# Performance work log

Hardware: AMD Instinct MI355X
Metric: run time of the kernel (lower is better)

Reference implementation:

```python
import jax, jax.numpy as jnp
import numpy as np

MAXTIME = 1406073600
MINTIME = 832550400
SPAN = 10000
TIME_EMB = 100
N_GATE = 8
NUM_INTEREST = 4
DIM = 64
SEQ = 256
BATCH = 1024
ALPHA = 0.1
PI = 3.14159  # matches the literal in the source


def _build_time_table():
    # TimeEncoder: interleaved sin/cos positional table over time buckets.
    n = MAXTIME // SPAN + 3
    pos = np.arange(n, dtype=np.float64)[:, None]
    div = np.exp(np.arange(TIME_EMB // 2, dtype=np.float64) * -(np.log(10000.0) / TIME_EMB))[None, :]
    te = np.zeros((n, TIME_EMB), dtype=np.float32)
    te[:, 0::2] = np.sin(pos * div)
    te[:, 1::2] = np.cos(pos * div)
    return jnp.asarray(te)

_TIME_TABLE = _build_time_table()


def _time_encode(t):
    idx = (t / SPAN).astype(jnp.int32)
    return _TIME_TABLE[idx - jnp.min(idx)]


def setup_inputs() -> dict:
    key = jax.random.key(0)
    ks = jax.random.split(key, 11)
    B, S, D, NI, G = BATCH, SEQ, DIM, NUM_INTEREST, N_GATE
    item_his_emb = jax.random.normal(ks[0], (B, S, D), jnp.float32)
    item_eb = jax.random.normal(ks[1], (B, D), jnp.float32)
    # query times near maxtime, history times strictly earlier -> positive deltas
    t_batch = MAXTIME - 1e6 * jax.random.uniform(ks[2], (B,), jnp.float32)
    t_his = MINTIME + (MAXTIME - MINTIME - 1e6) * jax.random.uniform(ks[3], (B, S), jnp.float32)
    mask = (jax.random.uniform(ks[4], (B, S)) > 0.3).astype(jnp.float32)
    W1 = jax.random.normal(ks[5], (3 * TIME_EMB, 100), jnp.float32) / np.sqrt(3 * TIME_EMB)
    b1 = jnp.zeros((100,), jnp.float32)
    W2 = jax.random.normal(ks[6], (100, 1), jnp.float32) * 0.1
    b2 = jnp.zeros((1,), jnp.float32)
    phase = 100000.0 * jax.random.uniform(ks[7], (1, 1, G), jnp.float32)
    tao = 86400.0 * jnp.array([[[1, 2, 7, 14, 30, 60, 365, 730]]], jnp.float32)
    ratio = 0.3 * jax.random.uniform(ks[8], (1, 1, G), jnp.float32)
    gate_emb = jax.random.normal(ks[9], (1, D, G), jnp.float32)
    w_bilinear = jax.random.normal(ks[10], (S, NI * D, D), jnp.float32)
    return {"item_his_emb": item_his_emb, "item_eb": item_eb, "t_batch": t_batch,
            "t_his": t_his, "mask": mask, "W1": W1, "b1": b1, "W2": W2, "b2": b2,
            "phase": phase, "tao": tao, "ratio": ratio, "gate_emb": gate_emb,
            "w_bilinear": w_bilinear, "ta": 2}


def reference(item_his_emb, item_eb, t_batch, t_his, mask, W1, b1, W2, b2,
              phase, tao, ratio, gate_emb, w_bilinear, ta):
    B, S, D = item_his_emb.shape
    NI = NUM_INTEREST
    # --- time factor ---
    t_tiled = jnp.broadcast_to(t_batch[:, None], (B, S))
    time_feature = jnp.concatenate([_time_encode(t_tiled), _time_encode(t_his),
                                    _time_encode(t_tiled - t_his)], axis=2)  # [B,S,300]
    hidden1 = jax.nn.relu(time_feature @ W1 + b1)
    t_factor = jnp.transpose(jax.nn.sigmoid(hidden1 @ W2 + b2), (0, 2, 1))  # [B,1,S]
    # --- circadian gate factor ---
    phi = jnp.mod(t_his[:, :, None] - phase, tao) / tao  # [B,S,G]
    gate = jnp.where(phi < ratio, jnp.maximum(jnp.sin(PI * phi / ratio), 0.0), ALPHA * phi)
    gate_ratio = jax.nn.softmax(jnp.einsum('bsd,dg->bsg', item_his_emb, gate_emb[0]), axis=2) * gate
    g_factor = jnp.sum(gate_ratio, axis=2)[:, None, :]  # [B,1,S]
    reg1 = jnp.linalg.norm(t_factor)
    reg2 = jnp.linalg.norm(ratio) + jnp.linalg.norm(phase) / 100000.0
    # ta == 2 branch
    loss_reg = 0.1 * reg1 + 1.0 * reg2 + 1.0 / reg1 + 0.1 / reg2
    factor = jnp.broadcast_to(t_factor + g_factor, (B, NI, S))
    # --- bilinear_type == 2 projection ---
    item_emb_hat = jnp.einsum('skd,bsd->bsk', w_bilinear, item_his_emb)  # [B,S,NI*D]
    item_emb_hat = item_emb_hat.reshape(B, S, NI, D).transpose(0, 2, 1, 3)  # [B,NI,S,D]
    hat_iter = jax.lax.stop_gradient(item_emb_hat)
    # --- dynamic routing, 3 iterations ---
    cw = jnp.zeros((B, NI, S), item_his_emb.dtype)
    amask = mask[:, None, :]
    cap = None
    for i in range(3):
        sw = jax.nn.softmax(cw, axis=1)           # softmax over interests
        sw = jnp.where(amask == 0, 0.0, sw)
        src = hat_iter if i < 2 else item_emb_hat
        cap = jnp.einsum('bks,bksd->bkd', sw, src)  # [B,NI,D]
        n2 = jnp.sum(cap * cap, axis=-1, keepdims=True)
        cap = (n2 / (1.0 + n2) / jnp.sqrt(n2 + 1e-9)) * cap  # squash
        if i < 2:
            delta = jnp.einsum('bksd,bkd->bks', hat_iter, cap) * factor
            cw = cw + delta
    interest_capsule = cap  # [B,NI,D]
    # --- hard readout ---
    atten = jax.nn.softmax(jnp.einsum('bkd,bd->bk', interest_capsule, item_eb), axis=1)
    readout = interest_capsule[jnp.arange(B), jnp.argmax(atten, axis=1)]  # [B,D]
    return interest_capsule, readout, loss_reg
```

## Files before the change

kernel.cpp:

```cpp
#include <hip/hip_runtime.h>
#include <math.h>
#include <limits.h>

#define BB 1024
#define SS 256
#define DD 64
#define NI 4
#define NG 8
#define TE_N 100
#define PMAX 57420
#define ROWP 100
#define TPB 16

typedef _Float16 half8 __attribute__((ext_vector_type(8)));
typedef _Float16 half4 __attribute__((ext_vector_type(4)));
typedef float f32x4 __attribute__((ext_vector_type(4)));

#define OFF_FTH   ((size_t)0)
#define OFF_FDF   ((size_t)PMAX*ROWP)
#define OFF_GTB   ((size_t)2*PMAX*ROWP)
#define OFF_FAC   (OFF_GTB + (size_t)BB*ROWP)
#define OFF_SCAL  (OFF_FAC + (size_t)BB*SS)
#define OFF_HAT   (OFF_SCAL + 32)

__device__ inline float dpp_add_xor1(float x){
    int i = __builtin_bit_cast(int, x);
    int p = __builtin_amdgcn_update_dpp(i, i, 0xB1, 0xF, 0xF, true);
    return x + __builtin_bit_cast(float, p);
}
__device__ inline float dpp_add_xor2(float x){
    int i = __builtin_bit_cast(int, x);
    int p = __builtin_amdgcn_update_dpp(i, i, 0x4E, 0xF, 0xF, true);
    return x + __builtin_bit_cast(float, p);
}
__device__ inline float swz_add_xor16(float x){
    int i = __builtin_bit_cast(int, x);
    int p = __builtin_amdgcn_ds_swizzle(i, 0x401F);
    return x + __builtin_bit_cast(float, p);
}

__global__ void k_init(float* ws){
    if (threadIdx.x == 0){
        int* mi = (int*)(ws + OFF_SCAL);
        mi[0] = INT_MAX; mi[1] = INT_MAX; mi[2] = INT_MAX;
        ws[OFF_SCAL + 4] = 0.0f;
    }
}

__global__ void k_min(const float* __restrict__ tb, const float* __restrict__ th, float* ws){
    int gid = blockIdx.x * blockDim.x + threadIdx.x;
    int stride = gridDim.x * blockDim.x;
    int m0 = INT_MAX, m1 = INT_MAX, m2 = INT_MAX;
    for (int i = gid; i < BB*SS; i += stride){
        float t  = th[i];
        float t2 = tb[i >> 8];
        int i1 = (int)(t / 10000.0f);
        int i2 = (int)((t2 - t) / 10000.0f);
        m1 = min(m1, i1);
        m2 = min(m2, i2);
    }
    if (gid < BB) m0 = (int)(tb[gid] / 10000.0f);
    #pragma unroll
    for (int off = 1; off < 64; off <<= 1){
        m0 = min(m0, __shfl_xor(m0, off));
        m1 = min(m1, __shfl_xor(m1, off));
        m2 = min(m2, __shfl_xor(m2, off));
    }
    if ((threadIdx.x & 63) == 0){
        int* mi = (int*)(ws + OFF_SCAL);
        atomicMin(mi + 0, m0);
        atomicMin(mi + 1, m1);
        atomicMin(mi + 2, m2);
    }
}

__global__ void k_tables(const float* __restrict__ W1, float* ws){
    int pbase = blockIdx.x * TPB;
    int t = threadIdx.x;
    __shared__ float te[TPB][TE_N];
    for (int idx = t; idx < TPB*50; idx += 128){
        int pp = idx / 50, h = idx - pp*50;
        double div = exp((double)h * -0.09210340371976184);
        double a = (double)(pbase + pp) * div;
        te[pp][2*h]   = (float)sin(a);
        te[pp][2*h+1] = (float)cos(a);
    }
    __syncthreads();
    if (t < TE_N){
        float a1[TPB], a2[TPB];
        #pragma unroll
        for (int pp = 0; pp < TPB; pp++){ a1[pp] = 0.f; a2[pp] = 0.f; }
        for (int i = 0; i < TE_N; i++){
            float w1v = W1[(100+i)*100 + t];
            float w2v = W1[(200+i)*100 + t];
            #pragma unroll
            for (int pp = 0; pp < TPB; pp++){
                float v = te[pp][i];
                a1[pp] += v * w1v;
                a2[pp] += v * w2v;
            }
        }
        for (int pp = 0; pp < TPB; pp++){
            int p = pbase + pp;
            if (p < PMAX){
                ws[OFF_FTH + (size_t)p*ROWP + t] = a1[pp];
                ws[OFF_FDF + (size_t)p*ROWP + t] = a2[pp];
            }
        }
    }
}

__global__ void k_gtb(const float* __restrict__ tb, const float* __restrict__ W1,
                      const float* __restrict__ b1, float* ws){
    int b = blockIdx.x;
    int t = threadIdx.x;
    const int* mi = (const int*)(ws + OFF_SCAL);
    int p = (int)(tb[b] / 10000.0f) - mi[0];
    __shared__ float te[TE_N];
    if (t < TE_N/2){
        double div = exp((double)t * -0.09210340371976184);
        double a = (double)p * div;
        te[2*t]   = (float)sin(a);
        te[2*t+1] = (float)cos(a);
    }
    __syncthreads();
    if (t < TE_N){
        float a1 = b1[t];
        for (int i = 0; i < TE_N; i++) a1 += te[i] * W1[i*100 + t];
        ws[OFF_GTB + (size_t)b*ROWP + t] = a1;
    }
}

__global__ void __launch_bounds__(256) k_factor(const float* __restrict__ tbatch,
                         const float* __restrict__ th_, const float* __restrict__ W2,
                         const float* __restrict__ b2, float* ws){
    int b  = blockIdx.x >> 1;
    int sh = blockIdx.x & 1;
    int t  = threadIdx.x;
    int lane = t & 63, wv = t >> 6;
    __shared__ float sgtb[TE_N];
    if (t < TE_N) sgtb[t] = ws[OFF_GTB + (size_t)b*ROWP + t];
    __syncthreads();

    bool tail = (lane < 36);
    float w2a = W2[lane];
    float w2b = tail ? W2[64 + lane] : 0.f;
    float ga  = sgtb[lane];
    float gb  = tail ? sgtb[64 + lane] : 0.f;
    float bias = b2[0];

    int sbase = sh*128 + wv*32;
    const int* mi = (const int*)(ws + OFF_SCAL);
    int pth = 0, pdf = 0;
    if (lane < 32){
        float thv = th_[(size_t)b*SS + sbase + lane];
        float tbv = tbatch[b];
        pth = (int)(thv / 10000.0f) - mi[1];
        pdf = (int)((tbv - thv) / 10000.0f) - mi[2];
        pth = min(max(pth, 0), PMAX-1);
        pdf = min(max(pdf, 0), PMAX-1);
    }

    float tfkeep = 0.f;
    float r1acc  = 0.f;
    #pragma unroll 4
    for (int i = 0; i < 32; i++){
        int p1 = __shfl(pth, i);
        int p2 = __shfl(pdf, i);
        const float* r1 = ws + OFF_FTH + (size_t)p1*ROWP;
        const float* r2 = ws + OFF_FDF + (size_t)p2*ROWP;
        float a  = r1[lane];
        float c  = r2[lane];
        float a2 = tail ? r1[64 + lane] : 0.f;
        float c2 = tail ? r2[64 + lane] : 0.f;
        float h = fmaxf(ga + a + c, 0.f) * w2a;
        if (tail) h += fmaxf(gb + a2 + c2, 0.f) * w2b;
        #pragma unroll
        for (int off = 1; off < 64; off <<= 1) h += __shfl_xor(h, off);
        float tf = 1.f / (1.f + expf(-(h + bias)));
        if (lane == i){ tfkeep = tf; r1acc += tf*tf; }
    }
    if (lane < 32) ws[OFF_FAC + (size_t)b*SS + sbase + lane] = tfkeep;
    #pragma unroll
    for (int off = 1; off < 64; off <<= 1) r1acc += __shfl_xor(r1acc, off);
    if (lane == 0) atomicAdd(ws + OFF_SCAL + 4, r1acc);
}

__global__ void __launch_bounds__(256) k_gate(const float* __restrict__ X,
      const float* __restrict__ th_, const float* __restrict__ phase,
      const float* __restrict__ tao, const float* __restrict__ ratio,
      const float* __restrict__ ge, float* ws){
    __shared__ float sge[NG][DD];
    int t = threadIdx.x;
    for (int i = t; i < DD*NG; i += 256) sge[i & 7][i >> 3] = ge[i];
    __syncthreads();
    int gid = blockIdx.x * 256 + t;

    float lg[NG];
    #pragma unroll
    for (int g = 0; g < NG; g++) lg[g] = 0.f;
    const float4* xr = (const float4*)(X + (size_t)gid*DD);
    #pragma unroll 4
    for (int dc = 0; dc < 16; dc++){
        float4 xv = xr[dc];
        #pragma unroll
        for (int g = 0; g < NG; g++){
            lg[g] += xv.x*sge[g][dc*4+0] + xv.y*sge[g][dc*4+1]
                   + xv.z*sge[g][dc*4+2] + xv.w*sge[g][dc*4+3];
        }
    }
    float mx = lg[0];
    #pragma unroll
    for (int g = 1; g < NG; g++) mx = fmaxf(mx, lg[g]);
    float thv = th_[gid];
    float es = 0.f, gf = 0.f;
    #pragma unroll
    for (int g = 0; g < NG; g++){
        float e = expf(lg[g] - mx);
        es += e;
        float phv = fmodf(thv - phase[g], tao[g]) / tao[g];
        float gv = (phv < ratio[g]) ? fmaxf(sinf(3.14159f*phv/ratio[g]), 0.f) : 0.1f*phv;
        gf += e * gv;
    }
    ws[OFF_FAC + gid] += gf / es;
}

__global__ void __launch_bounds__(512, 2)
k_hat(const float* __restrict__ X, const float* __restrict__ Wb,
      float* __restrict__ hat, int b0, int nb){
    int btile = blockIdx.x;
    int s     = blockIdx.y;
    int t     = threadIdx.x;
    int rows = nb - btile*64; if (rows > 64) rows = 64;

    __shared__ _Float16 lds[40960];

    const float* xbase = X + ((size_t)(b0 + btile*64)*SS + s)*DD;
    #pragma unroll
    for (int i = 0; i < 2; i++){
        int q = t + 512*i;
        int r = q >> 4, jf = q & 15;
        float4 v;
        if (r < rows) v = *(const float4*)(xbase + (size_t)r*SS*DD + jf*4);
        else { v.x = 0.f; v.y = 0.f; v.z = 0.f; v.w = 0.f; }
        half4 h, l;
        h.x = (_Float16)v.x; h.y = (_Float16)v.y; h.z = (_Float16)v.z; h.w = (_Float16)v.w;
        l.x = (_Float16)(v.x - (float)h.x); l.y = (_Float16)(v.y - (float)h.y);
        l.z = (_Float16)(v.z - (float)h.z); l.w = (_Float16)(v.w - (float)h.w);
        int bt = r >> 4, rowin = r & 15;
        int j0 = jf*4;
        int kk = j0 >> 5, jb = (j0 & 31) >> 3, e0 = j0 & 7;
        int lane = rowin + 16*jb;
        int base = ((bt*2 + kk)*2)*512 + lane*8 + e0;
        *(half4*)(lds + base)       = h;
        *(half4*)(lds + base + 512) = l;
    }
    const float* wbase = Wb + (size_t)s*16384;
    #pragma unroll
    for (int i = 0; i < 8; i++){
        int q = t + 512*i;
        int kd = q >> 4, jf = q & 15;
        float4 v = *(const float4*)(wbase + kd*64 + jf*4);
        half4 h, l;
        h.x = (_Float16)v.x; h.y = (_Float16)v.y; h.z = (_Float16)v.z; h.w = (_Float16)v.w;
        l.x = (_Float16)(v.x - (float)h.x); l.y = (_Float16)(v.y - (float)h.y);
        l.z = (_Float16)(v.z - (float)h.z); l.w = (_Float16)(v.w - (float)h.w);
        int kdt = kd >> 4, rowin = kd & 15;
        int j0 = jf*4;
        int kk = j0 >> 5, jb = (j0 & 31) >> 3, e0 = j0 & 7;
        int lane = rowin + 16*jb;
        int base = 8192 + ((kdt*2 + kk)*2)*512 + lane*8 + e0;
        *(half4*)(lds + base)       = h;
        *(half4*)(lds + base + 512) = l;
    }
    __syncthreads();

    int w    = t >> 6;
    int lane = t & 63;
    int wbt  = w >> 1;
    int kdh  = w & 1;

    half8 a[2][2];
    #pragma unroll
    for (int kk = 0; kk < 2; kk++)
        #pragma unroll
        for (int hl = 0; hl < 2; hl++)
            a[kk][hl] = *(half8*)(lds + ((wbt*2 + kk)*2 + hl)*512 + lane*8);

    int brow = (lane >> 4) * 4;
    int bcol = lane & 15;

    #pragma unroll
    for (int kdti = 0; kdti < 8; kdti++){
        int kdt = kdh*8 + kdti;
        const _Float16* wb0 = lds + 8192 + ((kdt*2 + 0)*2)*512 + lane*8;
        const _Float16* wb1 = lds + 8192 + ((kdt*2 + 1)*2)*512 + lane*8;
        half8 bh0 = *(half8*)(wb0);
        half8 bl0 = *(half8*)(wb0 + 512);
        half8 bh1 = *(half8*)(wb1);
        half8 bl1 = *(half8*)(wb1 + 512);
        f32x4 acc = {0.f, 0.f, 0.f, 0.f};
        acc = __builtin_amdgcn_mfma_f32_16x16x32_f16(a[0][0], bh0, acc, 0, 0, 0);
        acc = __builtin_amdgcn_mfma_f32_16x16x32_f16(a[0][0], bl0, acc, 0, 0, 0);
        acc = __builtin_amdgcn_mfma_f32_16x16x32_f16(a[0][1], bh0, acc, 0, 0, 0);
        acc = __builtin_amdgcn_mfma_f32_16x16x32_f16(a[1][0], bh1, acc, 0, 0, 0);
        acc = __builtin_amdgcn_mfma_f32_16x16x32_f16(a[1][0], bl1, acc, 0, 0, 0);
        acc = __builtin_amdgcn_mfma_f32_16x16x32_f16(a[1][1], bh1, acc, 0, 0, 0);
        int kd = kdt*16 + bcol;
        #pragma unroll
        for (int r = 0; r < 4; r++){
            int rl = wbt*16 + brow + r;
            if (rl < rows)
                hat[((size_t)(btile*64 + rl)*SS + s)*256 + kd] = acc[r];
        }
    }
}

__global__ void __launch_bounds__(1024) k_route(const float* __restrict__ eb,
                                                const float* __restrict__ mask_,
                                                const float* __restrict__ ws,
                                                const float* __restrict__ hat,
                                                float* __restrict__ out, int b0){
    int bl = blockIdx.x;
    int b = b0 + bl;
    int t = threadIdx.x;
    int lane = t & 63, wv = t >> 6;
    int k = (lane >> 2) & 3;
    int s_local = (lane & 3) | (((lane >> 4) & 3) << 2);
    int s = wv * 16 + s_local;
    __shared__ float part[16][4][64];
    __shared__ float capl[4][68];
    __shared__ float logits[4];
    __shared__ int kms;

    float hat_r[64];
    const float4* hsrc = (const float4*)(hat + (size_t)bl*65536 + ((size_t)s*4 + k)*64);
    #pragma unroll
    for (int jc = 0; jc < 16; jc++){
        float4 v = hsrc[jc];
        hat_r[4*jc] = v.x; hat_r[4*jc+1] = v.y; hat_r[4*jc+2] = v.z; hat_r[4*jc+3] = v.w;
    }
    float fac = ws[OFF_FAC + (size_t)b*SS + s];
    float mk = mask_[(size_t)b*SS + s];
    float cw = 0.f;
    float capv = 0.f;

    for (int it = 0; it < 3; ++it){
        float sw;
        if (it == 0){
            sw = (mk == 0.f) ? 0.f : 0.25f;
        } else {
            float m = fmaxf(cw, __shfl_xor(cw, 4)); m = fmaxf(m, __shfl_xor(m, 8));
            float e = expf(cw - m);
            float ssum = e + __shfl_xor(e, 4); ssum += __shfl_xor(ssum, 8);
            sw = (mk == 0.f) ? 0.f : (e / ssum);
        }

        #pragma unroll
        for (int c = 0; c < 4; c++){
            float tmp[16];
            #pragma unroll
            for (int i = 0; i < 16; i++) tmp[i] = sw * hat_r[c*16 + i];
            #pragma unroll
            for (int i = 0; i < 16; i++) tmp[i] = dpp_add_xor1(tmp[i]);
            #pragma unroll
            for (int i = 0; i < 16; i++) tmp[i] = dpp_add_xor2(tmp[i]);
            #pragma unroll
            for (int i = 0; i < 16; i++) tmp[i] = swz_add_xor16(tmp[i]);
            #pragma unroll
            for (int i = 0; i < 16; i++) tmp[i] += __shfl_xor(tmp[i], 32);
            if ((lane & 0x33) == 0){
                float* dst = &part[wv][lane >> 2][c*16];
                #pragma unroll
                for (int i = 0; i < 4; i++)
                    ((float4*)dst)[i] = make_float4(tmp[4*i], tmp[4*i+1], tmp[4*i+2], tmp[4*i+3]);
            }
        }
        __syncthreads();
        if (t < 256){
            int k2 = t >> 6, d = t & 63;
            float cp = 0.f;
            #pragma unroll
            for (int w2 = 0; w2 < 16; w2++) cp += part[w2][k2][d];
            float q = cp * cp;
            #pragma unroll
            for (int msk = 1; msk < 64; msk <<= 1) q += __shfl_xor(q, msk);
            float sc = q / ((1.f + q) * sqrtf(q + 1e-9f));
            capv = sc * cp;
            capl[k2][d] = capv;
        }
        __syncthreads();
        if (it < 2){
            const float4* cp4 = (const float4*)&capl[k][0];
            float dot = 0.f;
            #pragma unroll
            for (int jc = 0; jc < 16; jc++){
                float4 v = cp4[jc];
                dot += hat_r[4*jc]*v.x + hat_r[4*jc+1]*v.y + hat_r[4*jc+2]*v.z + hat_r[4*jc+3]*v.w;
            }
            cw += dot * fac;
        }
        __syncthreads();
    }

    if (t < 256){
        int k2 = t >> 6, d = t & 63;
        out[(size_t)b*256 + t] = capv;
        float qq = capv * eb[(size_t)b*DD + d];
        #pragma unroll
        for (int msk = 1; msk < 64; msk <<= 1) qq += __shfl_xor(qq, msk);
        if (lane == 0) logits[k2] = qq;
    }
    __syncthreads();
    if (t == 0){
        float best = logits[0]; int km = 0;
        for (int kk = 1; kk < 4; kk++) if (logits[kk] > best){ best = logits[kk]; km = kk; }
        kms = km;
    }
    __syncthreads();
    if (t < 64) out[(size_t)BB*256 + (size_t)b*64 + t] = capl[kms][t];
}

__global__ void k_final(const float* __restrict__ phase, const float* __restrict__ ratio,
                        float* ws, float* __restrict__ out){
    if (threadIdx.x == 0){
        float r2a = 0.f, r2b = 0.f;
        for (int g = 0; g < NG; g++){ r2a += ratio[g]*ratio[g]; r2b += phase[g]*phase[g]; }
        float reg2 = sqrtf(r2a) + sqrtf(r2b) / 100000.0f;
        float reg1 = sqrtf(ws[OFF_SCAL + 4]);
        out[(size_t)BB*256 + (size_t)BB*64] = 0.1f*reg1 + reg2 + 1.0f/reg1 + 0.1f/reg2;
    }
}

extern "C" void kernel_launch(void* const* d_in, const int* in_sizes, int n_in,
                              void* d_out, int out_size, void* d_ws, size_t ws_size,
                              hipStream_t stream){
    const float* Xh = (const float*)d_in[0];
    const float* eb = (const float*)d_in[1];
    const float* tb = (const float*)d_in[2];
    const float* th = (const float*)d_in[3];
    const float* mk = (const float*)d_in[4];
    const float* W1 = (const float*)d_in[5];
    const float* b1 = (const float*)d_in[6];
    const float* W2 = (const float*)d_in[7];
    const float* b2 = (const float*)d_in[8];
    const float* ph = (const float*)d_in[9];
    const float* ta = (const float*)d_in[10];
    const float* ra = (const float*)d_in[11];
    const float* ge = (const float*)d_in[12];
    const float* wb = (const float*)d_in[13];
    float* out = (float*)d_out;
    float* ws  = (float*)d_ws;

    hipLaunchKernelGGL(k_init,   dim3(1),    dim3(64),  0, stream, ws);
    hipLaunchKernelGGL(k_min,    dim3(256),  dim3(256), 0, stream, tb, th, ws);
    hipLaunchKernelGGL(k_tables, dim3((PMAX+TPB-1)/TPB), dim3(128), 0, stream, W1, ws);
    hipLaunchKernelGGL(k_gtb,    dim3(BB),   dim3(128), 0, stream, tb, W1, b1, ws);
    hipLaunchKernelGGL(k_factor, dim3(2*BB), dim3(256), 0, stream, tb, th, W2, b2, ws);
    hipLaunchKernelGGL(k_gate,   dim3(BB),   dim3(256), 0, stream, Xh, th, ph, ta, ra, ge, ws);

    long wfloats  = (long)(ws_size / sizeof(float));
    long hatavail = wfloats - (long)OFF_HAT;
    int CH = (int)(hatavail / 65536);
    if (CH > BB) CH = BB;
    if (CH >= 128) CH &= ~127;
    if (CH < 1)  CH = 1;
    float* hatbuf = ws + OFF_HAT;
    for (int c0 = 0; c0 < BB; c0 += CH){
        int nb = BB - c0; if (nb > CH) nb = CH;
        int nbt = (nb + 63) / 64;
        hipLaunchKernelGGL(k_hat,   dim3(nbt, 256), dim3(512),  0, stream, Xh, wb, hatbuf, c0, nb);
        hipLaunchKernelGGL(k_route, dim3(nb),       dim3(1024), 0, stream, eb, mk, ws, hatbuf, out, c0);
    }
    hipLaunchKernelGGL(k_final, dim3(1), dim3(64), 0, stream, ph, ra, ws, out);
}
```

Before: 493.6 us.

## Bucket-sort factor work items by table index for gather locality

Adds histogram, scan and scatter kernels that sort the (batch, seq) time-factor work items into 64 buckets by the history-time table row. The factor kernel then processes the sorted records, with interleaved block ordering, and gathers per-batch GTB rows. The aim is to make the large FTH-table gathers more cache-local. It also switches the 64-lane reductions to DPP and swizzle. This adds three extra launches, workspace for the records, and per-item GTB gathers, and shrinks the hat buffer space.

```diff
diff --git a/kernel.cpp b/kernel.cpp
--- a/kernel.cpp
+++ b/kernel.cpp
@@ -21,7 +21,9 @@
 #define OFF_GTB   ((size_t)2*PMAX*ROWP)
 #define OFF_FAC   (OFF_GTB + (size_t)BB*ROWP)
 #define OFF_SCAL  (OFF_FAC + (size_t)BB*SS)
-#define OFF_HAT   (OFF_SCAL + 32)
+#define OFF_REC   (OFF_SCAL + 160)
+#define OFF_SREC  (OFF_REC + (size_t)BB*SS*2)
+#define OFF_HAT   (OFF_SREC + (size_t)BB*SS*2)
 
 __device__ inline float dpp_add_xor1(float x){
     int i = __builtin_bit_cast(int, x);
@@ -40,11 +42,13 @@
 }
 
 __global__ void k_init(float* ws){
-    if (threadIdx.x == 0){
-        int* mi = (int*)(ws + OFF_SCAL);
-        mi[0] = INT_MAX; mi[1] = INT_MAX; mi[2] = INT_MAX;
+    int t = threadIdx.x;
+    int* ib = (int*)(ws + OFF_SCAL);
+    if (t == 0){
+        ib[0] = INT_MAX; ib[1] = INT_MAX; ib[2] = INT_MAX;
         ws[OFF_SCAL + 4] = 0.0f;
     }
+    if (t >= 8 && t < 136) ib[t] = 0;
 }
 
 __global__ void k_min(const float* __restrict__ tb, const float* __restrict__ th, float* ws){
@@ -131,56 +135,95 @@
     }
 }
 
-__global__ void __launch_bounds__(256) k_factor(const float* __restrict__ tbatch,
-                         const float* __restrict__ th_, const float* __restrict__ W2,
+__global__ void __launch_bounds__(256) k_hist(const float* __restrict__ tb,
+                                              const float* __restrict__ th, float* ws){
+    __shared__ int lh[64];
+    int t = threadIdx.x;
+    if (t < 64) lh[t] = 0;
+    __syncthreads();
+    int gid = blockIdx.x*256 + t;
+    int b = gid >> 8;
+    const int* mi = (const int*)(ws + OFF_SCAL);
+    float thv = th[gid], tbv = tb[b];
+    int p1 = (int)(thv / 10000.0f) - mi[1];
+    int p2 = (int)((tbv - thv) / 10000.0f) - mi[2];
+    p1 = min(max(p1, 0), PMAX-1);
+    p2 = min(max(p2, 0), PMAX-1);
+    ((uint2*)(ws + OFF_REC))[gid] = make_uint2((unsigned)p1 | ((unsigned)p2 << 16), (unsigned)gid);
+    atomicAdd(&lh[p1 >> 10], 1);
+    __syncthreads();
+    if (t < 64 && lh[t]) atomicAdd((int*)(ws + OFF_SCAL) + 8 + t, lh[t]);
+}
+
+__global__ void k_scan(float* ws){
+    if (threadIdx.x == 0){
+        int* g   = (int*)(ws + OFF_SCAL) + 8;
+        int* cur = (int*)(ws + OFF_SCAL) + 72;
+        int acc = 0;
+        for (int i = 0; i < 64; i++){ cur[i] = acc; acc += g[i]; }
+    }
+}
+
+__global__ void __launch_bounds__(256) k_scatter(float* ws){
+    __shared__ int lh[64], lbase[64];
+    int t = threadIdx.x;
+    if (t < 64) lh[t] = 0;
+    __syncthreads();
+    int gid = blockIdx.x*256 + t;
+    uint2 r = ((const uint2*)(ws + OFF_REC))[gid];
+    int bkt = (int)(r.x & 0xFFFFu) >> 10;
+    int myloc = atomicAdd(&lh[bkt], 1);
+    __syncthreads();
+    if (t < 64 && lh[t]) lbase[t] = atomicAdd((int*)(ws + OFF_SCAL) + 72 + t, lh[t]);
+    __syncthreads();
+    ((uint2*)(ws + OFF_SREC))[lbase[bkt] + myloc] = r;
+}
+
+__global__ void __launch_bounds__(256) k_factor2(const float* __restrict__ W2,
                          const float* __restrict__ b2, float* ws){
-    int b  = blockIdx.x >> 1;
-    int sh = blockIdx.x & 1;
-    int t  = threadIdx.x;
+    int t = threadIdx.x;
     int lane = t & 63, wv = t >> 6;
-    __shared__ float sgtb[TE_N];
-    if (t < TE_N) sgtb[t] = ws[OFF_GTB + (size_t)b*ROWP + t];
-    __syncthreads();
+    int bid = blockIdx.x;
+    int sbid = (bid & 7)*256 + (bid >> 3);
+    int pbase = sbid*128 + wv*32;
 
     bool tail = (lane < 36);
     float w2a = W2[lane];
     float w2b = tail ? W2[64 + lane] : 0.f;
-    float ga  = sgtb[lane];
-    float gb  = tail ? sgtb[64 + lane] : 0.f;
     float bias = b2[0];
 
-    int sbase = sh*128 + wv*32;
-    const int* mi = (const int*)(ws + OFF_SCAL);
-    int pth = 0, pdf = 0;
+    unsigned rx = 0, ry = 0;
     if (lane < 32){
-        float thv = th_[(size_t)b*SS + sbase + lane];
-        float tbv = tbatch[b];
-        pth = (int)(thv / 10000.0f) - mi[1];
-        pdf = (int)((tbv - thv) / 10000.0f) - mi[2];
-        pth = min(max(pth, 0), PMAX-1);
-        pdf = min(max(pdf, 0), PMAX-1);
-    }
-
-    float tfkeep = 0.f;
-    float r1acc  = 0.f;
+        uint2 r = ((const uint2*)(ws + OFF_SREC))[pbase + lane];
+        rx = r.x; ry = r.y;
+    }
+
+    float tfkeep = 0.f, r1acc = 0.f;
     #pragma unroll 4
     for (int i = 0; i < 32; i++){
-        int p1 = __shfl(pth, i);
-        int p2 = __shfl(pdf, i);
+        unsigned rxi = (unsigned)__shfl((int)rx, i);
+        unsigned ryi = (unsigned)__shfl((int)ry, i);
+        int p1 = (int)(rxi & 0xFFFFu);
+        int p2 = (int)(rxi >> 16);
+        int bi = (int)(ryi >> 8);
         const float* r1 = ws + OFF_FTH + (size_t)p1*ROWP;
         const float* r2 = ws + OFF_FDF + (size_t)p2*ROWP;
-        float a  = r1[lane];
-        float c  = r2[lane];
-        float a2 = tail ? r1[64 + lane] : 0.f;
-        float c2 = tail ? r2[64 + lane] : 0.f;
-        float h = fmaxf(ga + a + c, 0.f) * w2a;
-        if (tail) h += fmaxf(gb + a2 + c2, 0.f) * w2b;
-        #pragma unroll
-        for (int off = 1; off < 64; off <<= 1) h += __shfl_xor(h, off);
+        const float* rg = ws + OFF_GTB + (size_t)bi*ROWP;
+        float a = r1[lane];
+        float c = r2[lane];
+        float g = rg[lane];
+        float h = fmaxf(g + a + c, 0.f) * w2a;
+        if (tail) h += fmaxf(rg[64+lane] + r1[64+lane] + r2[64+lane], 0.f) * w2b;
+        h = dpp_add_xor1(h);
+        h = dpp_add_xor2(h);
+        h += __shfl_xor(h, 4);
+        h += __shfl_xor(h, 8);
+        h = swz_add_xor16(h);
+        h += __shfl_xor(h, 32);
         float tf = 1.f / (1.f + expf(-(h + bias)));
-        if (lane == i){ tfkeep = tf; r1acc += tf*tf; }
-    }
-    if (lane < 32) ws[OFF_FAC + (size_t)b*SS + sbase + lane] = tfkeep;
+        if (lane == i){ tfkeep = tf; r1acc = tf*tf; }
+    }
+    if (lane < 32) ws[OFF_FAC + ry] = tfkeep;
     #pragma unroll
     for (int off = 1; off < 64; off <<= 1) r1acc += __shfl_xor(r1acc, off);
     if (lane == 0) atomicAdd(ws + OFF_SCAL + 4, r1acc);
@@ -452,12 +495,15 @@
     float* out = (float*)d_out;
     float* ws  = (float*)d_ws;
 
-    hipLaunchKernelGGL(k_init,   dim3(1),    dim3(64),  0, stream, ws);
-    hipLaunchKernelGGL(k_min,    dim3(256),  dim3(256), 0, stream, tb, th, ws);
-    hipLaunchKernelGGL(k_tables, dim3((PMAX+TPB-1)/TPB), dim3(128), 0, stream, W1, ws);
-    hipLaunchKernelGGL(k_gtb,    dim3(BB),   dim3(128), 0, stream, tb, W1, b1, ws);
-    hipLaunchKernelGGL(k_factor, dim3(2*BB), dim3(256), 0, stream, tb, th, W2, b2, ws);
-    hipLaunchKernelGGL(k_gate,   dim3(BB),   dim3(256), 0, stream, Xh, th, ph, ta, ra, ge, ws);
+    hipLaunchKernelGGL(k_init,    dim3(1),    dim3(256), 0, stream, ws);
+    hipLaunchKernelGGL(k_min,     dim3(256),  dim3(256), 0, stream, tb, th, ws);
+    hipLaunchKernelGGL(k_tables,  dim3((PMAX+TPB-1)/TPB), dim3(128), 0, stream, W1, ws);
+    hipLaunchKernelGGL(k_gtb,     dim3(BB),   dim3(128), 0, stream, tb, W1, b1, ws);
+    hipLaunchKernelGGL(k_hist,    dim3(BB),   dim3(256), 0, stream, tb, th, ws);
+    hipLaunchKernelGGL(k_scan,    dim3(1),    dim3(64),  0, stream, ws);
+    hipLaunchKernelGGL(k_scatter, dim3(BB),   dim3(256), 0, stream, ws);
+    hipLaunchKernelGGL(k_factor2, dim3(2*BB), dim3(256), 0, stream, W2, b2, ws);
+    hipLaunchKernelGGL(k_gate,    dim3(BB),   dim3(256), 0, stream, Xh, th, ph, ta, ra, ge, ws);
 
     long wfloats  = (long)(ws_size / sizeof(float));
     long hatavail = wfloats - (long)OFF_HAT;
```

Measured after the change: 522.6 us. 1.06x slower.
